# Optimization experiments

Measured on AMD Instinct MI355X. Metric: run time of the kernel, lower is better.

## Reference

```python
import jax, jax.numpy as jnp
import numpy as np

MEM_DIM, H, W = 1024, 16, 16
HW = H * W
N_TOKENS, BATCH = 8192, 8
C1, C2, EPS = 0.01, 0.03, 1e-8


def setup_inputs() -> dict:
    key = jax.random.key(0)
    ks = jax.random.split(key, 5)
    std_w = 1.0 / np.sqrt(HW)
    return {
        "input_tokens": jax.random.normal(ks[0], (N_TOKENS, BATCH, HW), dtype=jnp.float32),
        "memory": jax.random.normal(ks[1], (MEM_DIM, H, W), dtype=jnp.float32) * 0.1,
        "Wq": jax.random.normal(ks[2], (HW, HW), dtype=jnp.float32) * std_w,
        "Wk": jax.random.normal(ks[3], (HW, HW), dtype=jnp.float32) * std_w,
        "Wv": jax.random.normal(ks[4], (HW, HW), dtype=jnp.float32) * std_w,
    }


def _ssim(q, k):
    # q: [N, HW], k: [M, HW] -> ssim: [N, M]
    qm = jnp.mean(q, axis=1, keepdims=True)          # [N,1]
    km = jnp.mean(k, axis=1, keepdims=True)          # [M,1]
    qv = jnp.var(q, axis=1, ddof=1, keepdims=True)   # torch.var unbiased
    kv = jnp.var(k, axis=1, ddof=1, keepdims=True)
    cov = ((q - qm) @ (k - km).T) / (HW - 1)         # [N,M]
    mean_prod = qm @ km.T                            # [N,M]
    numerator = (2.0 * mean_prod + C1) * (2.0 * cov + C2)
    denominator = (qm ** 2 + km.T ** 2 + C1) * (qv + kv.T + C2)
    return numerator / (denominator + EPS)


def reference(input_tokens, memory, Wq, Wk, Wv):
    Nt, B, F = input_tokens.shape
    x = input_tokens.reshape(Nt * B, HW)             # [N, HW]
    q = x @ Wq.T                                     # Linear(bias=False): x @ W^T
    m = memory.reshape(MEM_DIM, HW)
    k = m @ Wk.T
    v = m @ Wv.T
    ssim = _ssim(q, k)                               # [N, MEM_DIM]
    att = jax.nn.softmax(ssim, axis=1)
    out = (att @ v).reshape(Nt, B, F)
    return out
```

## Files before the change

kernel.cpp:

```cpp
#include <hip/hip_runtime.h>
#include <math.h>

typedef __attribute__((ext_vector_type(8)))  short bf16x8;
typedef __attribute__((ext_vector_type(16))) float f32x16;
typedef __attribute__((ext_vector_type(4)))  float f32x4;
typedef __attribute__((ext_vector_type(4)))  unsigned uint4v;

#define MFMA32(a, b, c) __builtin_amdgcn_mfma_f32_32x32x16_bf16((a), (b), (c), 0, 0, 0)

namespace {
constexpr int HWF   = 256;
constexpr int MEMD  = 1024;
constexpr int NROWS = 65536;
constexpr int TM    = 128;
constexpr int NT    = MEMD / 32;
constexpr int THREADS = 256;
constexpr float C1v  = 0.01f;
constexpr float C2v  = 0.03f;
constexpr float EPSv = 1e-8f;
constexpr float RK   = 1.0f / 255.0f;

constexpr int KB0 = 0;
constexpr int KB1 = 16384;
constexpr int VB0 = 32768;
constexpr int VB1 = 49152;
constexpr int STATS = 65536;
constexpr int LRED  = STATS + 12288;
constexpr int SMEM_SZ = LRED + 512;
}

__device__ __forceinline__ short f2bf(float f) {
    union { float f; unsigned u; } v; v.f = f;
    unsigned r = v.u + 0x7fffu + ((v.u >> 16) & 1u);
    return (short)(r >> 16);
}

__device__ __forceinline__ unsigned cvtpk(float a, float b) {
    unsigned r;
    asm("v_cvt_pk_bf16_f32 %0, %1, %2" : "=v"(r) : "v"(a), "v"(b));
    return r;
}

__device__ __forceinline__ void plswap(unsigned &a, unsigned &b) {
#if defined(__has_builtin) && __has_builtin(__builtin_amdgcn_permlane32_swap)
    auto r = __builtin_amdgcn_permlane32_swap((int)a, (int)b, false, false);
    a = (unsigned)r[0]; b = (unsigned)r[1];
#else
    const bool h = (threadIdx.x & 32) != 0;
    const unsigned ax = (unsigned)__shfl_xor((int)a, 32);
    const unsigned bx = (unsigned)__shfl_xor((int)b, 32);
    const unsigned na = h ? bx : a;
    const unsigned nb = h ? b : ax;
    a = na; b = nb;
#endif
}

__device__ __forceinline__ void dma_tile16(const short* gbase, char* smem, int ldsbase,
                                           int wave, int lane) {
    const char* g = (const char*)gbase + wave * 4096 + lane * 16;
    char* l = smem + ldsbase + wave * 4096;
    #pragma unroll
    for (int i = 0; i < 4; ++i) {
        __builtin_amdgcn_global_load_lds(
            (const __attribute__((address_space(1))) unsigned int*)(g + i * 1024),
            (__attribute__((address_space(3))) unsigned int*)(l + i * 1024), 16, 0, 0);
    }
}

__global__ __launch_bounds__(256) void cast_wq(const float* __restrict__ W,
                                               short* __restrict__ Wb) {
    int i = blockIdx.x * 256 + threadIdx.x;
    Wb[i] = f2bf(W[i]);
}

__global__ __launch_bounds__(256) void prep_kv(
    const float* __restrict__ mem, const float* __restrict__ Wk,
    const float* __restrict__ Wv, short* __restrict__ kblob,
    short* __restrict__ vblob, float* __restrict__ sblob)
{
    __shared__ __align__(16) float mrows[4][HWF];
    __shared__ float redS[4][8];
    const int t = threadIdx.x, j0 = blockIdx.x * 4;

    for (int r = 0; r < 4; ++r) mrows[r][t] = mem[(size_t)(j0 + r) * HWF + t];
    __syncthreads();

    const float4* wk4 = reinterpret_cast<const float4*>(Wk + (size_t)t * HWF);
    const float4* wv4 = reinterpret_cast<const float4*>(Wv + (size_t)t * HWF);
    float kt[4] = {0, 0, 0, 0}, vt[4] = {0, 0, 0, 0};
    for (int i = 0; i < 64; ++i) {
        const float4 a = wk4[i], b = wv4[i];
        for (int r = 0; r < 4; ++r) {
            const float4 m = reinterpret_cast<const float4*>(mrows[r])[i];
            kt[r] += m.x * a.x + m.y * a.y + m.z * a.z + m.w * a.w;
            vt[r] += m.x * b.x + m.y * b.y + m.z * b.z + m.w * b.w;
        }
    }

    const int wv_ = t >> 6, ln = t & 63;
    {
        float s[4];
        for (int r = 0; r < 4; ++r) s[r] = kt[r];
        for (int m = 1; m < 64; m <<= 1)
            for (int r = 0; r < 4; ++r) s[r] += __shfl_xor(s[r], m);
        if (ln == 0) {
            for (int r = 0; r < 4; ++r) redS[wv_][r] = s[r];
        }
    }
    __syncthreads();
    float kmv[4], kc4[4];
    for (int r = 0; r < 4; ++r) {
        kmv[r] = (redS[0][r] + redS[1][r] + redS[2][r] + redS[3][r]) * (1.f / HWF);
        kc4[r] = kt[r] - kmv[r];
    }
    {
        float s[4];
        for (int r = 0; r < 4; ++r) s[r] = kc4[r] * kc4[r];
        for (int m = 1; m < 64; m <<= 1)
            for (int r = 0; r < 4; ++r) s[r] += __shfl_xor(s[r], m);
        if (ln == 0) {
            for (int r = 0; r < 4; ++r) redS[wv_][4 + r] = s[r];
        }
    }
    __syncthreads();
    float kvv[4];
    for (int r = 0; r < 4; ++r)
        kvv[r] = (redS[0][4+r] + redS[1][4+r] + redS[2][4+r] + redS[3][4+r]) * (1.f / (HWF - 1));

    const int jt = j0 >> 5;
    for (int r = 0; r < 4; ++r) {
        const int ro = (j0 & 31) + r;
        kblob[jt * 8192 + ro * 256 + (((t >> 3) ^ (ro & 7)) * 8) + (t & 7)] = f2bf(kc4[r]);
        vblob[jt * 8192 + t * 32 + (((ro >> 3) ^ (t & 3)) * 8) + (ro & 7)] = f2bf(vt[r]);
    }
    if (t < 4) {
        const int j = j0 + t;
        sblob[j]            = 2.f * kmv[t];
        sblob[1024 + j]     = kmv[t] * kmv[t] + C1v;
        sblob[2048 + j]     = kvv[t] + C2v;
    }
}

__global__ __launch_bounds__(THREADS, 2) void attn(
    const float* __restrict__ x, const short* __restrict__ wq_bf,
    const short* __restrict__ kblob, const short* __restrict__ vblob,
    const float* __restrict__ sblob, float* __restrict__ out)
{
    __shared__ __align__(16) char smem[SMEM_SZ];
    const int t = threadIdx.x, wave = t >> 6, lane = t & 63;
    const int lo = lane & 31, hi = lane >> 5;
    const int rg = wave;
    const int n0 = blockIdx.x * TM;
    const int tok = n0 + 32 * rg + lo;

    dma_tile16(kblob, smem, KB0, wave, lane);
    dma_tile16(vblob, smem, VB0, wave, lane);
    #pragma unroll
    for (int r = 0; r < 3; ++r) {
        __builtin_amdgcn_global_load_lds(
            (const __attribute__((address_space(1))) unsigned int*)
                ((const char*)sblob + r * 4096 + wave * 1024 + lane * 16),
            (__attribute__((address_space(3))) unsigned int*)
                (smem + STATS + r * 4096 + wave * 1024 + lane * 16), 16, 0, 0);
    }

    bf16x8 xB[16];
    {
        const float* xr = x + (size_t)tok * HWF;
        #pragma unroll
        for (int s = 0; s < 16; ++s) {
            const float4 a = *reinterpret_cast<const float4*>(xr + 16 * s + 8 * hi);
            const float4 b = *reinterpret_cast<const float4*>(xr + 16 * s + 8 * hi + 4);
            uint4v u;
            u[0] = cvtpk(a.x, a.y); u[1] = cvtpk(a.z, a.w);
            u[2] = cvtpk(b.x, b.y); u[3] = cvtpk(b.z, b.w);
            xB[s] = __builtin_bit_cast(bf16x8, u);
        }
    }

    f32x16 qD[8];
    #pragma unroll
    for (int nt = 0; nt < 8; ++nt) qD[nt] = (f32x16)(0.f);
    #pragma unroll
    for (int nt = 0; nt < 8; ++nt) {
        #pragma unroll
        for (int s = 0; s < 16; ++s) {
            const bf16x8 wa = *reinterpret_cast<const bf16x8*>(
                wq_bf + (size_t)(32 * nt + lo) * HWF + 16 * s + 8 * hi);
            qD[nt] = MFMA32(wa, xB[s], qD[nt]);
        }
    }

    float qs = 0.f, qss = 0.f;
    #pragma unroll
    for (int nt = 0; nt < 8; ++nt)
        #pragma unroll
        for (int i = 0; i < 16; ++i) {
            const float v = qD[nt][i];
            qs += v; qss = __builtin_fmaf(v, v, qss);
        }
    qs += __shfl_xor(qs, 32);
    qss += __shfl_xor(qss, 32);
    const float qm  = qs * (1.f / HWF);
    const float qv  = (qss - qs * qs * (1.f / HWF)) * (1.f / (HWF - 1));
    const float qm2 = qm * qm;

    bf16x8 qA[16];
    #pragma unroll
    for (int nt = 0; nt < 8; ++nt) {
        unsigned w[8];
        #pragma unroll
        for (int p = 0; p < 8; ++p) w[p] = cvtpk(qD[nt][2 * p], qD[nt][2 * p + 1]);
        #pragma unroll
        for (int h = 0; h < 2; ++h) {
            unsigned a0 = w[4 * h + 0], b0 = w[4 * h + 2];
            unsigned a1 = w[4 * h + 1], b1 = w[4 * h + 3];
            plswap(a0, b0); plswap(a1, b1);
            uint4v u; u[0] = a0; u[1] = a1; u[2] = b0; u[3] = b1;
            qA[2 * nt + h] = __builtin_bit_cast(bf16x8, u);
        }
    }

    f32x16 O4[8];
    #pragma unroll
    for (int ct = 0; ct < 8; ++ct) O4[ct] = (f32x16)(0.f);
    float l = 0.f;
    const int rx = (lo & 7);

    for (int jt = 0; jt < NT; ++jt) {
        const int cur = jt & 1;
        const int kb = cur ? KB1 : KB0, vb = cur ? VB1 : VB0;
        const int kbn = cur ? KB0 : KB1, vbn = cur ? VB0 : VB1;
        __syncthreads();
        if (jt + 1 < NT) {
            dma_tile16(kblob + (size_t)(jt + 1) * 8192, smem, kbn, wave, lane);
            dma_tile16(vblob + (size_t)(jt + 1) * 8192, smem, vbn, wave, lane);
        }

        f32x16 sacc = (f32x16)(0.f);
        __builtin_amdgcn_s_setprio(1);
        #pragma unroll
        for (int s = 0; s < 16; ++s) {
            const bf16x8 kfr = *reinterpret_cast<const bf16x8*>(
                smem + kb + lo * 512 + (((2 * s + hi) ^ rx) * 16));
            sacc = MFMA32(kfr, qA[s], sacc);
        }
        __builtin_amdgcn_s_setprio(0);

        unsigned pw[8];
        #pragma unroll
        for (int g = 0; g < 4; ++g) {
            const int soff = (32 * jt + 8 * g + 4 * hi) * 4;
            const f32x4 a4 = *reinterpret_cast<const f32x4*>(smem + STATS + soff);
            const f32x4 b4 = *reinterpret_cast<const f32x4*>(smem + STATS + 4096 + soff);
            const f32x4 c4 = *reinterpret_cast<const f32x4*>(smem + STATS + 8192 + soff);
            float pr[4];
            #pragma unroll
            for (int q = 0; q < 4; ++q) {
                const int i = 4 * g + q;
                const float cov2 = __builtin_fmaf(sacc[i], 2.f * RK, C2v);
                const float num  = __builtin_fmaf(a4[q], qm, C1v) * cov2;
                const float den  = __builtin_fmaf(qm2 + b4[q], qv + c4[q], EPSv);
                pr[q] = __expf(__fdividef(num, den));
                l += pr[q];
            }
            pw[2 * g]     = cvtpk(pr[0], pr[1]);
            pw[2 * g + 1] = cvtpk(pr[2], pr[3]);
        }

        #pragma unroll
        for (int h = 0; h < 2; ++h) {
            unsigned a0 = pw[4 * h + 0], b0 = pw[4 * h + 2];
            unsigned a1 = pw[4 * h + 1], b1 = pw[4 * h + 3];
            plswap(a0, b0); plswap(a1, b1);
            uint4v u; u[0] = a0; u[1] = a1; u[2] = b0; u[3] = b1;
            const bf16x8 pa = __builtin_bit_cast(bf16x8, u);
            __builtin_amdgcn_s_setprio(1);
            #pragma unroll
            for (int ct = 0; ct < 8; ++ct) {
                const bf16x8 vfr = *reinterpret_cast<const bf16x8*>(
                    smem + vb + (32 * ct + lo) * 64 + (((2 * h + hi) ^ (lo & 3)) * 16));
                O4[ct] = MFMA32(pa, vfr, O4[ct]);
            }
            __builtin_amdgcn_s_setprio(0);
        }
    }

    const float lf = l + __shfl_xor(l, 32);
    if (hi == 0)
        *reinterpret_cast<float*>(smem + LRED + (wave * 32 + lo) * 4) = lf;
    float rl[16];
    #pragma unroll
    for (int g = 0; g < 4; ++g) {
        const f32x4 lv = *reinterpret_cast<const f32x4*>(
            smem + LRED + wave * 128 + (8 * g + 4 * hi) * 4);
        rl[4 * g + 0] = 1.f / lv[0];
        rl[4 * g + 1] = 1.f / lv[1];
        rl[4 * g + 2] = 1.f / lv[2];
        rl[4 * g + 3] = 1.f / lv[3];
    }

    #pragma unroll
    for (int ct = 0; ct < 8; ++ct) {
        #pragma unroll
        for (int i = 0; i < 16; ++i) {
            const int row = 32 * rg + (i & 3) + 8 * (i >> 2) + 4 * hi;
            out[(size_t)(n0 + row) * HWF + 32 * ct + lo] = O4[ct][i] * rl[i];
        }
    }
}

extern "C" void kernel_launch(void* const* d_in, const int* in_sizes, int n_in,
                              void* d_out, int out_size, void* d_ws, size_t ws_size,
                              hipStream_t stream) {
    (void)in_sizes; (void)n_in; (void)out_size; (void)ws_size;
    const float* x   = (const float*)d_in[0];
    const float* mem = (const float*)d_in[1];
    const float* Wq  = (const float*)d_in[2];
    const float* Wk  = (const float*)d_in[3];
    const float* Wv  = (const float*)d_in[4];
    float* out = (float*)d_out;

    short* wq_bf = (short*)d_ws;
    short* kblob = wq_bf + 65536;
    short* vblob = kblob + (size_t)MEMD * HWF;
    float* sblob = (float*)(vblob + (size_t)MEMD * HWF);

    cast_wq<<<256, 256, 0, stream>>>(Wq, wq_bf);
    prep_kv<<<MEMD / 4, 256, 0, stream>>>(mem, Wk, Wv, kblob, vblob, sblob);
    attn<<<NROWS / TM, THREADS, 0, stream>>>(x, wq_bf, kblob, vblob, sblob, out);
}
```

Measured before the change: 259.1 us.

## Transpose Wk/Wv into scratch and restructure prep_kv for coalesced weight reads

Adds a prep_w kernel that transposes Wk and Wv into the output buffer, used as scratch, and merges the Wq bf16 cast into it. prep_kv then has each wave compute two memory rows with coalesced float4 loads of the transposed weights, wave-local reductions and vectorized blob stores, which removes the strided per-thread row reads and block-level syncs. The attention kernel splits the QK MFMA chain into two accumulators to shorten the dependency chain, and the V blob swizzle key changes to match the new store pattern. The output buffer is reused as scratch before attn overwrites it, which depends on stream ordering.

Result: slower. 328.5 us (+26.8%).

```diff
diff --git a/kernel.cpp b/kernel.cpp
--- a/kernel.cpp
+++ b/kernel.cpp
@@ -67,77 +67,128 @@
     }
 }
 
-__global__ __launch_bounds__(256) void cast_wq(const float* __restrict__ W,
-                                               short* __restrict__ Wb) {
-    int i = blockIdx.x * 256 + threadIdx.x;
-    Wb[i] = f2bf(W[i]);
+__global__ __launch_bounds__(256) void prep_w(
+    const float* __restrict__ Wq, const float* __restrict__ Wk,
+    const float* __restrict__ Wv, short* __restrict__ wq_bf,
+    float* __restrict__ WkT, float* __restrict__ WvT)
+{
+    __shared__ float tl[64][65];
+    const int b = blockIdx.x, t = threadIdx.x;
+    if (b < 32) {
+        const float* src = (b < 16) ? Wk : Wv;
+        float* dst = (b < 16) ? WkT : WvT;
+        const int tile = b & 15, tr0 = (tile >> 2) * 64, tc0 = (tile & 3) * 64;
+        #pragma unroll
+        for (int k2 = 0; k2 < 16; ++k2) {
+            const int lin = k2 * 256 + t, r = lin >> 6, c = lin & 63;
+            tl[r][c] = src[(size_t)(tr0 + r) * HWF + tc0 + c];
+        }
+        __syncthreads();
+        #pragma unroll
+        for (int k2 = 0; k2 < 16; ++k2) {
+            const int lin = k2 * 256 + t, c = lin >> 6, r = lin & 63;
+            dst[(size_t)(tc0 + c) * HWF + tr0 + r] = tl[r][c];
+        }
+    } else {
+        const int base = (b - 32) * 8192;
+        #pragma unroll
+        for (int k2 = 0; k2 < 32; ++k2) {
+            const int i = base + k2 * 256 + t;
+            wq_bf[i] = f2bf(Wq[i]);
+        }
+    }
 }
 
 __global__ __launch_bounds__(256) void prep_kv(
-    const float* __restrict__ mem, const float* __restrict__ Wk,
-    const float* __restrict__ Wv, short* __restrict__ kblob,
+    const float* __restrict__ mem, const float* __restrict__ WkT,
+    const float* __restrict__ WvT, short* __restrict__ kblob,
     short* __restrict__ vblob, float* __restrict__ sblob)
 {
-    __shared__ __align__(16) float mrows[4][HWF];
-    __shared__ float redS[4][8];
-    const int t = threadIdx.x, j0 = blockIdx.x * 4;
-
-    for (int r = 0; r < 4; ++r) mrows[r][t] = mem[(size_t)(j0 + r) * HWF + t];
+    __shared__ __align__(16) float mrows[8][HWF];
+    const int t = threadIdx.x, j0 = blockIdx.x * 8;
+    #pragma unroll
+    for (int k2 = 0; k2 < 8; ++k2) {
+        const int lin = k2 * 256 + t;
+        mrows[lin >> 8][lin & 255] = mem[(size_t)j0 * HWF + lin];
+    }
     __syncthreads();
 
-    const float4* wk4 = reinterpret_cast<const float4*>(Wk + (size_t)t * HWF);
-    const float4* wv4 = reinterpret_cast<const float4*>(Wv + (size_t)t * HWF);
-    float kt[4] = {0, 0, 0, 0}, vt[4] = {0, 0, 0, 0};
-    for (int i = 0; i < 64; ++i) {
-        const float4 a = wk4[i], b = wv4[i];
-        for (int r = 0; r < 4; ++r) {
-            const float4 m = reinterpret_cast<const float4*>(mrows[r])[i];
-            kt[r] += m.x * a.x + m.y * a.y + m.z * a.z + m.w * a.w;
-            vt[r] += m.x * b.x + m.y * b.y + m.z * b.z + m.w * b.w;
-        }
-    }
-
-    const int wv_ = t >> 6, ln = t & 63;
+    const int w = t >> 6, ln = t & 63;
+    const int ja = j0 + 2 * w, jb = ja + 1;
+    float ka[4] = {0,0,0,0}, kb_[4] = {0,0,0,0};
+    float va[4] = {0,0,0,0}, vb_[4] = {0,0,0,0};
+    const float4* wkT4 = reinterpret_cast<const float4*>(WkT) + ln;
+    const float4* wvT4 = reinterpret_cast<const float4*>(WvT) + ln;
+
+    for (int c4 = 0; c4 < 64; ++c4) {
+        const float4 m0 = reinterpret_cast<const float4*>(mrows[2 * w])[c4];
+        const float4 m1 = reinterpret_cast<const float4*>(mrows[2 * w + 1])[c4];
+        const float m0a[4] = {m0.x, m0.y, m0.z, m0.w};
+        const float m1a[4] = {m1.x, m1.y, m1.z, m1.w};
+        #pragma unroll
+        for (int e = 0; e < 4; ++e) {
+            const int c = 4 * c4 + e;
+            const float4 wk = wkT4[c * 64];
+            const float4 wv = wvT4[c * 64];
+            ka[0]  = __builtin_fmaf(m0a[e], wk.x, ka[0]);
+            ka[1]  = __builtin_fmaf(m0a[e], wk.y, ka[1]);
+            ka[2]  = __builtin_fmaf(m0a[e], wk.z, ka[2]);
+            ka[3]  = __builtin_fmaf(m0a[e], wk.w, ka[3]);
+            kb_[0] = __builtin_fmaf(m1a[e], wk.x, kb_[0]);
+            kb_[1] = __builtin_fmaf(m1a[e], wk.y, kb_[1]);
+            kb_[2] = __builtin_fmaf(m1a[e], wk.z, kb_[2]);
+            kb_[3] = __builtin_fmaf(m1a[e], wk.w, kb_[3]);
+            va[0]  = __builtin_fmaf(m0a[e], wv.x, va[0]);
+            va[1]  = __builtin_fmaf(m0a[e], wv.y, va[1]);
+            va[2]  = __builtin_fmaf(m0a[e], wv.z, va[2]);
+            va[3]  = __builtin_fmaf(m0a[e], wv.w, va[3]);
+            vb_[0] = __builtin_fmaf(m1a[e], wv.x, vb_[0]);
+            vb_[1] = __builtin_fmaf(m1a[e], wv.y, vb_[1]);
+            vb_[2] = __builtin_fmaf(m1a[e], wv.z, vb_[2]);
+            vb_[3] = __builtin_fmaf(m1a[e], wv.w, vb_[3]);
+        }
+    }
+
+    float sa = ka[0] + ka[1] + ka[2] + ka[3];
+    float sb = kb_[0] + kb_[1] + kb_[2] + kb_[3];
+    #pragma unroll
+    for (int m = 1; m < 64; m <<= 1) { sa += __shfl_xor(sa, m); sb += __shfl_xor(sb, m); }
+    const float kma = sa * (1.f / HWF), kmb = sb * (1.f / HWF);
+    float kca[4], kcb[4];
+    #pragma unroll
+    for (int e = 0; e < 4; ++e) { kca[e] = ka[e] - kma; kcb[e] = kb_[e] - kmb; }
+    float qa = kca[0]*kca[0] + kca[1]*kca[1] + kca[2]*kca[2] + kca[3]*kca[3];
+    float qb = kcb[0]*kcb[0] + kcb[1]*kcb[1] + kcb[2]*kcb[2] + kcb[3]*kcb[3];
+    #pragma unroll
+    for (int m = 1; m < 64; m <<= 1) { qa += __shfl_xor(qa, m); qb += __shfl_xor(qb, m); }
+    const float kva = qa * (1.f / (HWF - 1)), kvb = qb * (1.f / (HWF - 1));
+
+    const int jt = ja >> 5, roa = ja & 31, rob = jb & 31;
     {
-        float s[4];
-        for (int r = 0; r < 4; ++r) s[r] = kt[r];
-        for (int m = 1; m < 64; m <<= 1)
-            for (int r = 0; r < 4; ++r) s[r] += __shfl_xor(s[r], m);
-        if (ln == 0) {
-            for (int r = 0; r < 4; ++r) redS[wv_][r] = s[r];
-        }
-    }
-    __syncthreads();
-    float kmv[4], kc4[4];
-    for (int r = 0; r < 4; ++r) {
-        kmv[r] = (redS[0][r] + redS[1][r] + redS[2][r] + redS[3][r]) * (1.f / HWF);
-        kc4[r] = kt[r] - kmv[r];
-    }
-    {
-        float s[4];
-        for (int r = 0; r < 4; ++r) s[r] = kc4[r] * kc4[r];
-        for (int m = 1; m < 64; m <<= 1)
-            for (int r = 0; r < 4; ++r) s[r] += __shfl_xor(s[r], m);
-        if (ln == 0) {
-            for (int r = 0; r < 4; ++r) redS[wv_][4 + r] = s[r];
-        }
-    }
-    __syncthreads();
-    float kvv[4];
-    for (int r = 0; r < 4; ++r)
-        kvv[r] = (redS[0][4+r] + redS[1][4+r] + redS[2][4+r] + redS[3][4+r]) * (1.f / (HWF - 1));
-
-    const int jt = j0 >> 5;
-    for (int r = 0; r < 4; ++r) {
-        const int ro = (j0 & 31) + r;
-        kblob[jt * 8192 + ro * 256 + (((t >> 3) ^ (ro & 7)) * 8) + (t & 7)] = f2bf(kc4[r]);
-        vblob[jt * 8192 + t * 32 + (((ro >> 3) ^ (t & 3)) * 8) + (ro & 7)] = f2bf(vt[r]);
-    }
-    if (t < 4) {
-        const int j = j0 + t;
-        sblob[j]            = 2.f * kmv[t];
-        sblob[1024 + j]     = kmv[t] * kmv[t] + C1v;
-        sblob[2048 + j]     = kvv[t] + C2v;
+        const int chk = ln >> 1, off = 4 * (ln & 1);
+        short4 s4a, s4b;
+        s4a.x = f2bf(kca[0]); s4a.y = f2bf(kca[1]); s4a.z = f2bf(kca[2]); s4a.w = f2bf(kca[3]);
+        s4b.x = f2bf(kcb[0]); s4b.y = f2bf(kcb[1]); s4b.z = f2bf(kcb[2]); s4b.w = f2bf(kcb[3]);
+        *reinterpret_cast<short4*>(kblob + jt * 8192 + roa * 256 +
+                                   ((chk ^ (roa & 7)) * 8) + off) = s4a;
+        *reinterpret_cast<short4*>(kblob + jt * 8192 + rob * 256 +
+                                   ((chk ^ (rob & 7)) * 8) + off) = s4b;
+    }
+    #pragma unroll
+    for (int e = 0; e < 4; ++e) {
+        const int f = 4 * ln + e;
+        const int key = (f >> 1) & 3;
+        short2 s2; s2.x = f2bf(va[e]); s2.y = f2bf(vb_[e]);
+        *reinterpret_cast<short2*>(vblob + jt * 8192 + f * 32 +
+                                   (((roa >> 3) ^ key) * 8) + (roa & 7)) = s2;
+    }
+    if (ln == 0) {
+        sblob[ja]        = 2.f * kma;
+        sblob[1024 + ja] = kma * kma + C1v;
+        sblob[2048 + ja] = kva + C2v;
+        sblob[jb]        = 2.f * kmb;
+        sblob[1024 + jb] = kmb * kmb + C1v;
+        sblob[2048 + jb] = kvb + C2v;
     }
 }
 
@@ -226,6 +277,7 @@
     for (int ct = 0; ct < 8; ++ct) O4[ct] = (f32x16)(0.f);
     float l = 0.f;
     const int rx = (lo & 7);
+    const int vx = (lo >> 1) & 3;
 
     for (int jt = 0; jt < NT; ++jt) {
         const int cur = jt & 1;
@@ -237,13 +289,16 @@
             dma_tile16(vblob + (size_t)(jt + 1) * 8192, smem, vbn, wave, lane);
         }
 
-        f32x16 sacc = (f32x16)(0.f);
+        f32x16 sacc0 = (f32x16)(0.f), sacc1 = (f32x16)(0.f);
         __builtin_amdgcn_s_setprio(1);
         #pragma unroll
-        for (int s = 0; s < 16; ++s) {
-            const bf16x8 kfr = *reinterpret_cast<const bf16x8*>(
+        for (int s = 0; s < 16; s += 2) {
+            const bf16x8 k0 = *reinterpret_cast<const bf16x8*>(
                 smem + kb + lo * 512 + (((2 * s + hi) ^ rx) * 16));
-            sacc = MFMA32(kfr, qA[s], sacc);
+            const bf16x8 k1 = *reinterpret_cast<const bf16x8*>(
+                smem + kb + lo * 512 + (((2 * s + 2 + hi) ^ rx) * 16));
+            sacc0 = MFMA32(k0, qA[s], sacc0);
+            sacc1 = MFMA32(k1, qA[s + 1], sacc1);
         }
         __builtin_amdgcn_s_setprio(0);
 
@@ -258,7 +313,8 @@
             #pragma unroll
             for (int q = 0; q < 4; ++q) {
                 const int i = 4 * g + q;
-                const float cov2 = __builtin_fmaf(sacc[i], 2.f * RK, C2v);
+                const float sv = sacc0[i] + sacc1[i];
+                const float cov2 = __builtin_fmaf(sv, 2.f * RK, C2v);
                 const float num  = __builtin_fmaf(a4[q], qm, C1v) * cov2;
                 const float den  = __builtin_fmaf(qm2 + b4[q], qv + c4[q], EPSv);
                 pr[q] = __expf(__fdividef(num, den));
@@ -279,7 +335,7 @@
             #pragma unroll
             for (int ct = 0; ct < 8; ++ct) {
                 const bf16x8 vfr = *reinterpret_cast<const bf16x8*>(
-                    smem + vb + (32 * ct + lo) * 64 + (((2 * h + hi) ^ (lo & 3)) * 16));
+                    smem + vb + (32 * ct + lo) * 64 + (((2 * h + hi) ^ vx) * 16));
                 O4[ct] = MFMA32(pa, vfr, O4[ct]);
             }
             __builtin_amdgcn_s_setprio(0);
@@ -326,7 +382,10 @@
     short* vblob = kblob + (size_t)MEMD * HWF;
     float* sblob = (float*)(vblob + (size_t)MEMD * HWF);
 
-    cast_wq<<<256, 256, 0, stream>>>(Wq, wq_bf);
-    prep_kv<<<MEMD / 4, 256, 0, stream>>>(mem, Wk, Wv, kblob, vblob, sblob);
+    float* WkT = out;
+    float* WvT = out + 65536;
+
+    prep_w<<<40, 256, 0, stream>>>(Wq, Wk, Wv, wq_bf, WkT, WvT);
+    prep_kv<<<MEMD / 8, 256, 0, stream>>>(mem, WkT, WvT, kblob, vblob, sblob);
     attn<<<NROWS / TM, THREADS, 0, stream>>>(x, wq_bf, kblob, vblob, sblob, out);
 }
```

## Compute K/V projections with bf16 MFMA and vectorize weight casts

Applied to the files above, without the earlier changes.

Replaces the scalar fp32 prep kernel for the K and V projections with an MFMA-based kernel that uses bf16 weights. A single vectorized kernel now casts Wq, Wk and Wv, staging Wk/Wv in the output buffer as scratch. The V blob swizzle and the matching attention read pattern are changed to suit the new write layout. Memory is now rounded to bf16 before projection, and the variance uses the one-pass sum-of-squares formula, both of which cost some precision. The prep grid shrinks to 16 blocks, which leaves most of the GPU idle during that stage.

Measured after the change: 264.8 us. +2.2%, slower.

```diff
diff --git a/kernel.cpp b/kernel.cpp
--- a/kernel.cpp
+++ b/kernel.cpp
@@ -67,77 +67,105 @@
     }
 }
 
-__global__ __launch_bounds__(256) void cast_wq(const float* __restrict__ W,
-                                               short* __restrict__ Wb) {
-    int i = blockIdx.x * 256 + threadIdx.x;
-    Wb[i] = f2bf(W[i]);
-}
-
-__global__ __launch_bounds__(256) void prep_kv(
-    const float* __restrict__ mem, const float* __restrict__ Wk,
-    const float* __restrict__ Wv, short* __restrict__ kblob,
+__global__ __launch_bounds__(256) void cast_w(
+    const float* __restrict__ Wq, const float* __restrict__ Wk,
+    const float* __restrict__ Wv, short* __restrict__ wq_bf,
+    short* __restrict__ wk_bf, short* __restrict__ wv_bf)
+{
+    const int b = blockIdx.x, t = threadIdx.x;
+    const float* src = (b < 32) ? Wq : (b < 64) ? Wk : Wv;
+    short* dst = (b < 32) ? wq_bf : (b < 64) ? wk_bf : wv_bf;
+    const int i = (b & 31) * 2048 + t * 8;
+    const float4 a = *reinterpret_cast<const float4*>(src + i);
+    const float4 c = *reinterpret_cast<const float4*>(src + i + 4);
+    uint4v u;
+    u[0] = cvtpk(a.x, a.y); u[1] = cvtpk(a.z, a.w);
+    u[2] = cvtpk(c.x, c.y); u[3] = cvtpk(c.z, c.w);
+    *reinterpret_cast<uint4v*>(dst + i) = u;
+}
+
+__global__ __launch_bounds__(256) void prep_mfma(
+    const float* __restrict__ mem, const short* __restrict__ wk_bf,
+    const short* __restrict__ wv_bf, short* __restrict__ kblob,
     short* __restrict__ vblob, float* __restrict__ sblob)
 {
-    __shared__ __align__(16) float mrows[4][HWF];
-    __shared__ float redS[4][8];
-    const int t = threadIdx.x, j0 = blockIdx.x * 4;
-
-    for (int r = 0; r < 4; ++r) mrows[r][t] = mem[(size_t)(j0 + r) * HWF + t];
-    __syncthreads();
-
-    const float4* wk4 = reinterpret_cast<const float4*>(Wk + (size_t)t * HWF);
-    const float4* wv4 = reinterpret_cast<const float4*>(Wv + (size_t)t * HWF);
-    float kt[4] = {0, 0, 0, 0}, vt[4] = {0, 0, 0, 0};
-    for (int i = 0; i < 64; ++i) {
-        const float4 a = wk4[i], b = wv4[i];
-        for (int r = 0; r < 4; ++r) {
-            const float4 m = reinterpret_cast<const float4*>(mrows[r])[i];
-            kt[r] += m.x * a.x + m.y * a.y + m.z * a.z + m.w * a.w;
-            vt[r] += m.x * b.x + m.y * b.y + m.z * b.z + m.w * b.w;
-        }
-    }
-
-    const int wv_ = t >> 6, ln = t & 63;
+    const int t = threadIdx.x, wave = t >> 6, lane = t & 63;
+    const int lo = lane & 31, hi = lane >> 5;
+    const bool isV = blockIdx.x >= 8;
+    const int jb = (blockIdx.x & 7) * 128 + wave * 32;
+    const int j  = jb + lo;
+
+    bf16x8 mB[16];
     {
-        float s[4];
-        for (int r = 0; r < 4; ++r) s[r] = kt[r];
-        for (int m = 1; m < 64; m <<= 1)
-            for (int r = 0; r < 4; ++r) s[r] += __shfl_xor(s[r], m);
-        if (ln == 0) {
-            for (int r = 0; r < 4; ++r) redS[wv_][r] = s[r];
-        }
-    }
-    __syncthreads();
-    float kmv[4], kc4[4];
-    for (int r = 0; r < 4; ++r) {
-        kmv[r] = (redS[0][r] + redS[1][r] + redS[2][r] + redS[3][r]) * (1.f / HWF);
-        kc4[r] = kt[r] - kmv[r];
-    }
-    {
-        float s[4];
-        for (int r = 0; r < 4; ++r) s[r] = kc4[r] * kc4[r];
-        for (int m = 1; m < 64; m <<= 1)
-            for (int r = 0; r < 4; ++r) s[r] += __shfl_xor(s[r], m);
-        if (ln == 0) {
-            for (int r = 0; r < 4; ++r) redS[wv_][4 + r] = s[r];
-        }
-    }
-    __syncthreads();
-    float kvv[4];
-    for (int r = 0; r < 4; ++r)
-        kvv[r] = (redS[0][4+r] + redS[1][4+r] + redS[2][4+r] + redS[3][4+r]) * (1.f / (HWF - 1));
-
-    const int jt = j0 >> 5;
-    for (int r = 0; r < 4; ++r) {
-        const int ro = (j0 & 31) + r;
-        kblob[jt * 8192 + ro * 256 + (((t >> 3) ^ (ro & 7)) * 8) + (t & 7)] = f2bf(kc4[r]);
-        vblob[jt * 8192 + t * 32 + (((ro >> 3) ^ (t & 3)) * 8) + (ro & 7)] = f2bf(vt[r]);
-    }
-    if (t < 4) {
-        const int j = j0 + t;
-        sblob[j]            = 2.f * kmv[t];
-        sblob[1024 + j]     = kmv[t] * kmv[t] + C1v;
-        sblob[2048 + j]     = kvv[t] + C2v;
+        const float* mr = mem + (size_t)j * HWF;
+        #pragma unroll
+        for (int s = 0; s < 16; ++s) {
+            const float4 a = *reinterpret_cast<const float4*>(mr + 16 * s + 8 * hi);
+            const float4 b = *reinterpret_cast<const float4*>(mr + 16 * s + 8 * hi + 4);
+            uint4v u;
+            u[0] = cvtpk(a.x, a.y); u[1] = cvtpk(a.z, a.w);
+            u[2] = cvtpk(b.x, b.y); u[3] = cvtpk(b.z, b.w);
+            mB[s] = __builtin_bit_cast(bf16x8, u);
+        }
+    }
+
+    const short* W = isV ? wv_bf : wk_bf;
+    f32x16 D[8];
+    #pragma unroll
+    for (int nt = 0; nt < 8; ++nt) D[nt] = (f32x16)(0.f);
+    #pragma unroll
+    for (int nt = 0; nt < 8; ++nt) {
+        #pragma unroll
+        for (int s = 0; s < 16; ++s) {
+            const bf16x8 wa = *reinterpret_cast<const bf16x8*>(
+                W + (size_t)(32 * nt + lo) * HWF + 16 * s + 8 * hi);
+            D[nt] = MFMA32(wa, mB[s], D[nt]);
+        }
+    }
+
+    const int jt = jb >> 5, ro = lo;
+    if (!isV) {
+        float s = 0.f, ss = 0.f;
+        #pragma unroll
+        for (int nt = 0; nt < 8; ++nt)
+            #pragma unroll
+            for (int i = 0; i < 16; ++i) {
+                const float v = D[nt][i];
+                s += v; ss = __builtin_fmaf(v, v, ss);
+            }
+        s += __shfl_xor(s, 32);
+        ss += __shfl_xor(ss, 32);
+        const float km = s * (1.f / HWF);
+        const float kv = (ss - s * s * (1.f / HWF)) * (1.f / (HWF - 1));
+        #pragma unroll
+        for (int nt = 0; nt < 8; ++nt) {
+            #pragma unroll
+            for (int a = 0; a < 4; ++a) {
+                short4 q4;
+                q4.x = f2bf(D[nt][4 * a + 0] - km);
+                q4.y = f2bf(D[nt][4 * a + 1] - km);
+                q4.z = f2bf(D[nt][4 * a + 2] - km);
+                q4.w = f2bf(D[nt][4 * a + 3] - km);
+                *reinterpret_cast<short4*>(
+                    kblob + jt * 8192 + ro * 256 +
+                    (((4 * nt + a) ^ (ro & 7)) * 8) + 4 * hi) = q4;
+            }
+        }
+        if (hi == 0) {
+            sblob[j]        = 2.f * km;
+            sblob[1024 + j] = km * km + C1v;
+            sblob[2048 + j] = kv + C2v;
+        }
+    } else {
+        #pragma unroll
+        for (int nt = 0; nt < 8; ++nt) {
+            #pragma unroll
+            for (int i = 0; i < 16; ++i) {
+                const int f = 32 * nt + (i & 3) + 8 * (i >> 2) + 4 * hi;
+                vblob[jt * 8192 + f * 32 +
+                      (((ro >> 3) ^ ((f >> 1) & 3)) * 8) + (ro & 7)] = f2bf(D[nt][i]);
+            }
+        }
     }
 }
 
@@ -226,6 +254,7 @@
     for (int ct = 0; ct < 8; ++ct) O4[ct] = (f32x16)(0.f);
     float l = 0.f;
     const int rx = (lo & 7);
+    const int vx = (lo >> 1) & 3;
 
     for (int jt = 0; jt < NT; ++jt) {
         const int cur = jt & 1;
@@ -279,7 +308,7 @@
             #pragma unroll
             for (int ct = 0; ct < 8; ++ct) {
                 const bf16x8 vfr = *reinterpret_cast<const bf16x8*>(
-                    smem + vb + (32 * ct + lo) * 64 + (((2 * h + hi) ^ (lo & 3)) * 16));
+                    smem + vb + (32 * ct + lo) * 64 + (((2 * h + hi) ^ vx) * 16));
                 O4[ct] = MFMA32(pa, vfr, O4[ct]);
             }
             __builtin_amdgcn_s_setprio(0);
@@ -326,7 +355,10 @@
     short* vblob = kblob + (size_t)MEMD * HWF;
     float* sblob = (float*)(vblob + (size_t)MEMD * HWF);
 
-    cast_wq<<<256, 256, 0, stream>>>(Wq, wq_bf);
-    prep_kv<<<MEMD / 4, 256, 0, stream>>>(mem, Wk, Wv, kblob, vblob, sblob);
+    short* wk_bf = (short*)out;
+    short* wv_bf = wk_bf + 65536;
+
+    cast_w<<<96, 256, 0, stream>>>(Wq, Wk, Wv, wq_bf, wk_bf, wv_bf);
+    prep_mfma<<<16, 256, 0, stream>>>(mem, wk_bf, wv_bf, kblob, vblob, sblob);
     attn<<<NROWS / TM, THREADS, 0, stream>>>(x, wq_bf, kblob, vblob, sblob, out);
 }
```
